# Optimization experiments

Hardware: AMD Instinct MI355X
Metric: run time of the kernel (lower is better)

## Reference

```python
import jax, jax.numpy as jnp
import numpy as np

B, Q, WAY, SHOT, H, W, C = 2, 75, 5, 5, 10, 10, 640
NEIGHBOR_K = 5


def setup_inputs() -> dict:
    key = jax.random.key(0)
    k1, k2 = jax.random.split(key)
    input1 = jax.random.normal(k1, (B, Q, H, W, C), dtype=jnp.float32)
    # per the original unpacking: dim1=shot, dim2=way
    input2 = jax.random.normal(k2, (B, SHOT, WAY, H, W, C), dtype=jnp.float32)
    return {"input1": input1, "input2": input2, "neighbor_k": NEIGHBOR_K}


def reference(input1, input2, neighbor_k):
    # input1: [b, q_num, h, w, c] query local descriptors
    # input2: [b, shot, way, h, w, c] support local descriptors
    b, q_num, h, w, c = input1.shape
    _, shot, way, _, _, _ = input2.shape
    hw = h * w

    q = input1.reshape(b, q_num, hw, c)
    s = input2.reshape(b, way * shot, hw, c)

    # L2-normalize each local descriptor over channel dim
    q = q / jnp.linalg.norm(q, axis=-1, keepdims=True)
    s = s / jnp.linalg.norm(s, axis=-1, keepdims=True)

    # group support descriptors per class: [b, way, shot*hw, c]
    # (matches torch .view semantics on the contiguous flattened buffer)
    support = s.reshape(b, way, shot * hw, c)

    # cosine similarity between every query patch and every support patch
    # scores: [b, q_num, way, hw, shot*hw]
    scores = jnp.einsum('bqpc,bwsc->bqwps', q, support)

    # top-k nearest support descriptors per query patch, mean over k
    topv, _ = jax.lax.top_k(scores, neighbor_k)          # [b,q,way,hw,k]
    sim_local = jnp.sum(topv, axis=-1) / neighbor_k      # [b,q,way,hw]
    sim_way = jnp.sum(sim_local, axis=-1)                # [b,q,way]
    return sim_way
```

## Files before the change

### kernel.cpp

```cpp
#include <hip/hip_runtime.h>

#define QN    75
#define HWN   100
#define CN    640
#define NSUP  500
#define MROWS 7500
#define NQD   (2 * MROWS)
#define NSD   5000
#define NDESC (NQD + NSD)
#define MT    128
#define NT    256
#define BK    64
#define CST   272
#define BUFSZ 49152

typedef __attribute__((ext_vector_type(8))) __bf16 bf16x8;
typedef __attribute__((ext_vector_type(4))) float  f32x4;

#define GLDS(gp, lp) __builtin_amdgcn_global_load_lds(                        \
    (const __attribute__((address_space(1))) void*)(gp),                      \
    (__attribute__((address_space(3))) void*)(lp), 16, 0, 0)

static __device__ inline unsigned short f2bf(float f) {
    unsigned int u = __float_as_uint(f);
    u += 0x7fffu + ((u >> 16) & 1u);
    return (unsigned short)(u >> 16);
}

__global__ __launch_bounds__(256) void prep_kernel(const float* __restrict__ q,
                                                   const float* __restrict__ s,
                                                   unsigned short* __restrict__ qbf,
                                                   unsigned short* __restrict__ sbf) {
    int wave = (blockIdx.x * 256 + threadIdx.x) >> 6;
    int lane = threadIdx.x & 63;
    if (wave >= NDESC) return;
    const float* src = (wave < NQD) ? (q + (size_t)wave * CN)
                                    : (s + (size_t)(wave - NQD) * CN);
    unsigned short* dst = (wave < NQD) ? (qbf + (size_t)wave * CN)
                                       : (sbf + (size_t)(wave - NQD) * CN);
    float4 v[3];
    float ss = 0.f;
#pragma unroll
    for (int j = 0; j < 3; ++j) {
        int idx4 = lane + 64 * j;
        if (idx4 < CN / 4) {
            v[j] = *(const float4*)(src + idx4 * 4);
            ss = fmaf(v[j].x, v[j].x, ss);
            ss = fmaf(v[j].y, v[j].y, ss);
            ss = fmaf(v[j].z, v[j].z, ss);
            ss = fmaf(v[j].w, v[j].w, ss);
        }
    }
#pragma unroll
    for (int off = 32; off > 0; off >>= 1)
        ss += __shfl_xor(ss, off, 64);
    float inv = rsqrtf(ss);
#pragma unroll
    for (int j = 0; j < 3; ++j) {
        int idx4 = lane + 64 * j;
        if (idx4 < CN / 4) {
            ushort4 o;
            o.x = f2bf(v[j].x * inv);
            o.y = f2bf(v[j].y * inv);
            o.z = f2bf(v[j].z * inv);
            o.w = f2bf(v[j].w * inv);
            *(ushort4*)(dst + idx4 * 4) = o;
        }
    }
}

__global__ __launch_bounds__(512, 2) void mfma_kernel(const unsigned short* __restrict__ qbf,
                                                      const unsigned short* __restrict__ sbf,
                                                      float* __restrict__ part) {
    const int xcd = blockIdx.x & 7;
    const int idx = blockIdx.x >> 3;
    const int b   = xcd >> 2;
    const int mbq = xcd & 3;
    const int mbsz = (mbq < 3) ? 15 : 14;
    if (idx >= 10 * mbsz) return;
    const int g  = idx / (2 * mbsz);
    const int r_ = idx % (2 * mbsz);
    const int nc = r_ / mbsz;
    const int mb = mbq * 15 + (r_ % mbsz);
    const int bg = b * 5 + g;
    const int r0 = mb * MT;
    const int c0 = nc * NT;

    __shared__ __align__(16) char smem[2 * BUFSZ];
    float* Cst = (float*)smem;

    const int t    = threadIdx.x;
    const int lane = t & 63;
    const int wid  = t >> 6;
    const int h    = wid >> 2;
    const int colq = wid & 3;

    const unsigned short* qptr = qbf + (size_t)b * MROWS * CN;
    const unsigned short* sptr = sbf + (size_t)(b * 25 + g * 5) * HWN * CN;

    f32x4 acc[4][4];
#pragma unroll
    for (int mt = 0; mt < 4; ++mt)
#pragma unroll
        for (int nt = 0; nt < 4; ++nt)
            acc[mt][nt] = (f32x4)0.f;

    const int lx   = lane >> 3;
    const int ls   = lane & 7;
    const int gsrc = ls ^ lx;

    int ar0 = r0 + wid * 16 + lx;       if (ar0 > MROWS - 1) ar0 = MROWS - 1;
    int ar1 = r0 + wid * 16 + 8 + lx;   if (ar1 > MROWS - 1) ar1 = MROWS - 1;
    const int aoff0 = ar0 * CN + gsrc * 8;
    const int aoff1 = ar1 * CN + gsrc * 8;

    int boff[4];
#pragma unroll
    for (int c = 0; c < 4; ++c) {
        int col = c0 + wid * 32 + c * 8 + lx;
        if (col > NSUP - 1) col = NSUP - 1;
        boff[c] = col * CN + gsrc * 8;
    }

    const int q_ = lane >> 4;
    const int lr = lane & 15;
    const int sw = lr & 7;

#define STAGE(base, kk)                                                        \
    {                                                                          \
        char* ad = smem + (base) + wid * 2048;                                 \
        char* bd = smem + (base) + 16384 + wid * 4096;                         \
        GLDS(qptr + aoff0 + (kk), ad);                                         \
        GLDS(qptr + aoff1 + (kk), ad + 1024);                                  \
        GLDS(sptr + boff[0] + (kk), bd);                                       \
        GLDS(sptr + boff[1] + (kk), bd + 1024);                                \
        GLDS(sptr + boff[2] + (kk), bd + 2048);                                \
        GLDS(sptr + boff[3] + (kk), bd + 3072);                                \
    }

#define COMPUTE(base)                                                          \
    {                                                                          \
        const unsigned short* Al = (const unsigned short*)(smem + (base));     \
        const unsigned short* Bl = (const unsigned short*)(smem + (base) + 16384); \
        _Pragma("unroll")                                                      \
        for (int ks = 0; ks < 2; ++ks) {                                       \
            const int sl = ((ks * 4 + q_) ^ sw) * 8;                           \
            bf16x8 af[4];                                                      \
            _Pragma("unroll")                                                  \
            for (int mt = 0; mt < 4; ++mt)                                     \
                af[mt] = *(const bf16x8*)(Al + (h * 64 + mt * 16 + lr) * 64 + sl); \
            _Pragma("unroll")                                                  \
            for (int nt = 0; nt < 4; ++nt) {                                   \
                bf16x8 bfr = *(const bf16x8*)(Bl + (colq * 64 + nt * 16 + lr) * 64 + sl); \
                _Pragma("unroll")                                              \
                for (int mt = 0; mt < 4; ++mt)                                 \
                    acc[mt][nt] = __builtin_amdgcn_mfma_f32_16x16x32_bf16(af[mt], bfr, acc[mt][nt], 0, 0, 0); \
            }                                                                  \
        }                                                                      \
    }

    STAGE(0, 0);
    __syncthreads();
#pragma unroll 2
    for (int kt = 0; kt < 9; ++kt) {
        const int cb = (kt & 1) * BUFSZ;
        STAGE(BUFSZ - cb, (kt + 1) * BK);
        COMPUTE(cb);
        __syncthreads();
    }
    COMPUTE(BUFSZ);
#undef STAGE
#undef COMPUTE

    const int erow = t >> 4;
    const int es   = t & 15;
#define CE(a, b) { float hi_ = fmaxf(a, b), lo_ = fminf(a, b); a = hi_; b = lo_; }
#pragma unroll
    for (int mt = 0; mt < 4; ++mt) {
        __syncthreads();
#pragma unroll
        for (int nt = 0; nt < 4; ++nt)
#pragma unroll
            for (int e = 0; e < 4; ++e)
                Cst[(h * 16 + q_ * 4 + e) * CST + colq * 64 + nt * 16 + lr] = acc[mt][nt][e];
        __syncthreads();

        float t0 = -3.4e38f, t1 = -3.4e38f, t2 = -3.4e38f, t3 = -3.4e38f, t4 = -3.4e38f;
#pragma unroll
        for (int i = 0; i < 16; ++i) {
            int col = es + 16 * i;
            float v = (c0 + col < NSUP) ? Cst[erow * CST + col] : -3.4e38f;
            float hi;
            hi = fmaxf(t0, v); v = fminf(t0, v); t0 = hi;
            hi = fmaxf(t1, v); v = fminf(t1, v); t1 = hi;
            hi = fmaxf(t2, v); v = fminf(t2, v); t2 = hi;
            hi = fmaxf(t3, v); v = fminf(t3, v); t3 = hi;
            hi = fmaxf(t4, v); v = fminf(t4, v); t4 = hi;
        }
#pragma unroll
        for (int d = 1; d < 16; d <<= 1) {
            float b0 = __shfl_xor(t0, d, 64);
            float b1 = __shfl_xor(t1, d, 64);
            float b2 = __shfl_xor(t2, d, 64);
            float b3 = __shfl_xor(t3, d, 64);
            float b4 = __shfl_xor(t4, d, 64);
            t0 = fmaxf(t0, b4); t1 = fmaxf(t1, b3); t2 = fmaxf(t2, b2);
            t3 = fmaxf(t3, b1); t4 = fmaxf(t4, b0);
            CE(t0, t1); CE(t2, t3);
            CE(t1, t2); CE(t3, t4);
            CE(t0, t1); CE(t2, t3);
            CE(t1, t2); CE(t3, t4);
            CE(t0, t1); CE(t2, t3);
        }
        if (es == 0) {
            int patch = r0 + (erow >> 4) * 64 + mt * 16 + (erow & 15);
            if (patch < MROWS) {
                float* pp = part + ((size_t)(bg * MROWS + patch) * 2 + nc) * 5;
                pp[0] = t0; pp[1] = t1; pp[2] = t2; pp[3] = t3; pp[4] = t4;
            }
        }
    }
#undef CE
}

__global__ __launch_bounds__(256) void merge_kernel(const float* __restrict__ part,
                                                    float* __restrict__ out) {
    int w    = (blockIdx.x * 256 + threadIdx.x) >> 6;
    int lane = threadIdx.x & 63;
    if (w >= 750) return;
    int b  = w / 375, r = w % 375;
    int qi = r / 5,   g = r % 5;
    int bg = b * 5 + g;

    float sum = 0.f;
    for (int p = lane; p < HWN; p += 64) {
        int row = qi * HWN + p;
        const float* pp = part + (size_t)(bg * MROWS + row) * 10;
        float t0 = -3.4e38f, t1 = -3.4e38f, t2 = -3.4e38f, t3 = -3.4e38f, t4 = -3.4e38f;
#pragma unroll
        for (int j = 0; j < 10; ++j) {
            float v = pp[j], hi;
            hi = fmaxf(t0, v); v = fminf(t0, v); t0 = hi;
            hi = fmaxf(t1, v); v = fminf(t1, v); t1 = hi;
            hi = fmaxf(t2, v); v = fminf(t2, v); t2 = hi;
            hi = fmaxf(t3, v); v = fminf(t3, v); t3 = hi;
            hi = fmaxf(t4, v); v = fminf(t4, v); t4 = hi;
        }
        sum += (t0 + t1 + t2 + t3 + t4) * 0.2f;
    }
#pragma unroll
    for (int off = 32; off > 0; off >>= 1)
        sum += __shfl_xor(sum, off, 64);
    if (lane == 0) out[w] = sum;
}

extern "C" void kernel_launch(void* const* d_in, const int* in_sizes, int n_in,
                              void* d_out, int out_size, void* d_ws, size_t ws_size,
                              hipStream_t stream) {
    const float* in1 = (const float*)d_in[0];
    const float* in2 = (const float*)d_in[1];
    float* out = (float*)d_out;

    unsigned short* qbf  = (unsigned short*)d_ws;
    unsigned short* sbf  = qbf + (size_t)NQD * CN;
    float*          part = (float*)(sbf + (size_t)NSD * CN);

    prep_kernel<<<dim3(NDESC / 4), 256, 0, stream>>>(in1, in2, qbf, sbf);
    mfma_kernel<<<dim3(1200), 512, 0, stream>>>(qbf, sbf, part);
    merge_kernel<<<dim3(188), 256, 0, stream>>>(part, out);
}
```

Measured before the change: 169.1 us.

## Halve K-tile to 32 to shrink LDS and double blocks per CU

```diff
diff --git a/kernel.cpp b/kernel.cpp
--- a/kernel.cpp
+++ b/kernel.cpp
@@ -10,9 +10,9 @@
 #define NDESC (NQD + NSD)
 #define MT    128
 #define NT    256
-#define BK    64
+#define BK    32
+#define HBUF  24576
 #define CST   272
-#define BUFSZ 49152
 
 typedef __attribute__((ext_vector_type(8))) __bf16 bf16x8;
 typedef __attribute__((ext_vector_type(4))) float  f32x4;
@@ -69,7 +69,7 @@
     }
 }
 
-__global__ __launch_bounds__(512, 2) void mfma_kernel(const unsigned short* __restrict__ qbf,
+__global__ __launch_bounds__(512, 4) void mfma_kernel(const unsigned short* __restrict__ qbf,
                                                       const unsigned short* __restrict__ sbf,
                                                       float* __restrict__ part) {
     const int xcd = blockIdx.x & 7;
@@ -86,7 +86,7 @@
     const int r0 = mb * MT;
     const int c0 = nc * NT;
 
-    __shared__ __align__(16) char smem[2 * BUFSZ];
+    __shared__ __align__(16) char smem[2 * HBUF];
     float* Cst = (float*)smem;
 
     const int t    = threadIdx.x;
@@ -105,70 +105,63 @@
         for (int nt = 0; nt < 4; ++nt)
             acc[mt][nt] = (f32x4)0.f;
 
-    const int lx   = lane >> 3;
-    const int ls   = lane & 7;
-    const int gsrc = ls ^ lx;
-
-    int ar0 = r0 + wid * 16 + lx;       if (ar0 > MROWS - 1) ar0 = MROWS - 1;
-    int ar1 = r0 + wid * 16 + 8 + lx;   if (ar1 > MROWS - 1) ar1 = MROWS - 1;
-    const int aoff0 = ar0 * CN + gsrc * 8;
-    const int aoff1 = ar1 * CN + gsrc * 8;
-
-    int boff[4];
-#pragma unroll
-    for (int c = 0; c < 4; ++c) {
-        int col = c0 + wid * 32 + c * 8 + lx;
-        if (col > NSUP - 1) col = NSUP - 1;
-        boff[c] = col * CN + gsrc * 8;
-    }
+    const int lxr  = lane >> 2;
+    const int lg   = lane & 3;
+    const int gsrc = lg ^ ((lxr ^ (lxr >> 2)) & 3);
+
+    int ar = r0 + wid * 16 + lxr;            if (ar > MROWS - 1) ar = MROWS - 1;
+    const int aoff = ar * CN + gsrc * 8;
+    int bc0 = c0 + wid * 32 + lxr;           if (bc0 > NSUP - 1) bc0 = NSUP - 1;
+    int bc1 = c0 + wid * 32 + 16 + lxr;      if (bc1 > NSUP - 1) bc1 = NSUP - 1;
+    const int boff0 = bc0 * CN + gsrc * 8;
+    const int boff1 = bc1 * CN + gsrc * 8;
 
     const int q_ = lane >> 4;
     const int lr = lane & 15;
-    const int sw = lr & 7;
+    const int sl = (q_ ^ ((lr ^ (lr >> 2)) & 3)) * 8;
 
 #define STAGE(base, kk)                                                        \
     {                                                                          \
-        char* ad = smem + (base) + wid * 2048;                                 \
-        char* bd = smem + (base) + 16384 + wid * 4096;                         \
-        GLDS(qptr + aoff0 + (kk), ad);                                         \
-        GLDS(qptr + aoff1 + (kk), ad + 1024);                                  \
-        GLDS(sptr + boff[0] + (kk), bd);                                       \
-        GLDS(sptr + boff[1] + (kk), bd + 1024);                                \
-        GLDS(sptr + boff[2] + (kk), bd + 2048);                                \
-        GLDS(sptr + boff[3] + (kk), bd + 3072);                                \
+        char* ad = smem + (base) + wid * 1024;                                 \
+        char* bd = smem + (base) + 8192 + wid * 2048;                          \
+        GLDS(qptr + aoff  + (kk), ad);                                         \
+        GLDS(sptr + boff0 + (kk), bd);                                         \
+        GLDS(sptr + boff1 + (kk), bd + 1024);                                  \
     }
 
 #define COMPUTE(base)                                                          \
     {                                                                          \
         const unsigned short* Al = (const unsigned short*)(smem + (base));     \
-        const unsigned short* Bl = (const unsigned short*)(smem + (base) + 16384); \
+        const unsigned short* Bl = Al + 4096;                                  \
+        bf16x8 af[4];                                                          \
         _Pragma("unroll")                                                      \
-        for (int ks = 0; ks < 2; ++ks) {                                       \
-            const int sl = ((ks * 4 + q_) ^ sw) * 8;                           \
-            bf16x8 af[4];                                                      \
+        for (int mt = 0; mt < 4; ++mt)                                         \
+            af[mt] = *(const bf16x8*)(Al + (h * 64 + mt * 16 + lr) * 32 + sl); \
+        _Pragma("unroll")                                                      \
+        for (int nt = 0; nt < 4; ++nt) {                                       \
+            bf16x8 bfr = *(const bf16x8*)(Bl + (colq * 64 + nt * 16 + lr) * 32 + sl); \
             _Pragma("unroll")                                                  \
             for (int mt = 0; mt < 4; ++mt)                                     \
-                af[mt] = *(const bf16x8*)(Al + (h * 64 + mt * 16 + lr) * 64 + sl); \
-            _Pragma("unroll")                                                  \
-            for (int nt = 0; nt < 4; ++nt) {                                   \
-                bf16x8 bfr = *(const bf16x8*)(Bl + (colq * 64 + nt * 16 + lr) * 64 + sl); \
-                _Pragma("unroll")                                              \
-                for (int mt = 0; mt < 4; ++mt)                                 \
-                    acc[mt][nt] = __builtin_amdgcn_mfma_f32_16x16x32_bf16(af[mt], bfr, acc[mt][nt], 0, 0, 0); \
-            }                                                                  \
+                acc[mt][nt] = __builtin_amdgcn_mfma_f32_16x16x32_bf16(af[mt], bfr, acc[mt][nt], 0, 0, 0); \
         }                                                                      \
     }
 
     STAGE(0, 0);
     __syncthreads();
-#pragma unroll 2
-    for (int kt = 0; kt < 9; ++kt) {
-        const int cb = (kt & 1) * BUFSZ;
-        STAGE(BUFSZ - cb, (kt + 1) * BK);
-        COMPUTE(cb);
-        __syncthreads();
-    }
-    COMPUTE(BUFSZ);
+#pragma unroll 3
+    for (int k2 = 0; k2 < 9; ++k2) {
+        const int kk = k2 * 2;
+        STAGE(HBUF, (kk + 1) * BK);
+        COMPUTE(0);
+        __syncthreads();
+        STAGE(0, (kk + 2) * BK);
+        COMPUTE(HBUF);
+        __syncthreads();
+    }
+    STAGE(HBUF, 19 * BK);
+    COMPUTE(0);
+    __syncthreads();
+    COMPUTE(HBUF);
 #undef STAGE
 #undef COMPUTE
 
```

After: 163.8 us. 3.2% less time.
